# Kernel tuning notes

Hardware: AMD Instinct MI355X
Metric: run time of the kernel (lower is better)

Reference implementation:

```python
import jax, jax.numpy as jnp
import numpy as np

N = 50000      # num nodes
E = 500000     # num edges
R = 200        # num relations
DIN = 128      # ent input dim
DREL = 128     # relation dim
DOUT = 128     # output dim
SLOPE = 0.01   # torch LeakyReLU default negative_slope


def setup_inputs() -> dict:
    key = jax.random.key(0)
    ks = jax.random.split(key, 6)
    x = jax.random.normal(ks[0], (N, DIN), dtype=jnp.float32)
    relation_embedding = jax.random.normal(ks[1], (R, DREL), dtype=jnp.float32)
    edge_index = jax.random.randint(ks[2], (2, E), 0, N, dtype=jnp.int32)
    edge_type = jax.random.randint(ks[3], (E,), 0, R, dtype=jnp.int32)
    # Linear weights (xavier-ish scale), stored as [in, out] for x @ W
    W1 = jax.random.normal(ks[4], (2 * DIN + DREL, DOUT), dtype=jnp.float32) * 0.05
    b1 = jnp.zeros((DOUT,), dtype=jnp.float32)
    w2 = jax.random.normal(ks[5], (DOUT,), dtype=jnp.float32) * 0.05
    return {"x": x, "relation_embedding": relation_embedding, "W1": W1,
            "b1": b1, "w2": w2, "edge_index": edge_index, "edge_type": edge_type}


def reference(x, relation_embedding, W1, b1, w2, edge_index, edge_type):
    src, dst = edge_index[0], edge_index[1]
    n = x.shape[0]
    # gather + concat: [E, 2*DIN + DREL]
    triple = jnp.concatenate([x[src], x[dst], relation_embedding[edge_type]], axis=1)
    c = triple @ W1 + b1                         # [E, DOUT]
    b = jax.nn.leaky_relu(c @ w2, SLOPE)         # [E] attention logits
    # per-destination (segment) softmax — stable, fully vectorized
    seg_max = jax.ops.segment_max(b, dst, num_segments=n)
    ex = jnp.exp(b - seg_max[dst])
    denom = jax.ops.segment_sum(ex, dst, num_segments=n)
    alpha = ex / denom[dst]                      # [E]
    # weighted message scatter-add (dropout p=0 / eval -> identity)
    out = jax.ops.segment_sum(c * alpha[:, None], dst, num_segments=n)  # [N, DOUT]
    # final_layer=False -> leaky_relu on output
    return jax.nn.leaky_relu(out, SLOPE)
```

## Files before the change

kernel.cpp:

```cpp
#include <hip/hip_runtime.h>
#include <math.h>

#define SLOPE 0.01f
#define CHUNK_SHIFT 13
#define CHUNK_SZ (1 << CHUNK_SHIFT)
#define MAXWORDS 12544

using bf16x8 = __attribute__((ext_vector_type(8))) short;
using f32x4  = __attribute__((ext_vector_type(4))) float;

__device__ __forceinline__ unsigned short f2bf(float f) {
  unsigned int u = __float_as_uint(f);
  unsigned int r = 0x7FFFu + ((u >> 16) & 1u);
  return (unsigned short)((u + r) >> 16);
}
__device__ __forceinline__ float bflo(unsigned int v) {
  return __uint_as_float(v << 16);
}
__device__ __forceinline__ float bfhi(unsigned int v) {
  return __uint_as_float(v & 0xFFFF0000u);
}
__device__ __forceinline__ bf16x8 pack8(float4 a, float4 b) {
  bf16x8 r;
  r[0] = (short)f2bf(a.x); r[1] = (short)f2bf(a.y);
  r[2] = (short)f2bf(a.z); r[3] = (short)f2bf(a.w);
  r[4] = (short)f2bf(b.x); r[5] = (short)f2bf(b.y);
  r[6] = (short)f2bf(b.z); r[7] = (short)f2bf(b.w);
  return r;
}

__global__ __launch_bounds__(1024) void front(
    const float* __restrict__ W1, unsigned short* __restrict__ WT,
    const float* __restrict__ rel, const float* __restrict__ b1,
    const float* __restrict__ w2,
    unsigned short* __restrict__ Crelbf, float* __restrict__ pC, int n_rel,
    const int* __restrict__ dsts, unsigned int* __restrict__ cntg,
    unsigned char* __restrict__ rank8, int E, int words, int CB, int WB) {
  __shared__ __align__(16) unsigned int smem[MAXWORDS];
  int b = blockIdx.x;
  int tid = threadIdx.x;
  if (b < CB) {
    for (int w = tid; w < words; w += 1024) smem[w] = 0;
    __syncthreads();
    int base = b << CHUNK_SHIFT;
    int lim = E - base; if (lim > CHUNK_SZ) lim = CHUNK_SZ;
    for (int k = tid; k < lim; k += 1024) {
      int dn = dsts[base + k];
      unsigned int sh = 8u * (dn & 3);
      unsigned int old = atomicAdd(&smem[dn >> 2], 1u << sh);
      rank8[base + k] = (unsigned char)((old >> sh) & 0xFFu);
    }
    __syncthreads();
    unsigned int* dstp = cntg + (size_t)b * words;
    for (int w = tid; w < words; w += 1024) dstp[w] = smem[w];
  } else if (b < CB + WB) {
    int i = (b - CB) * 1024 + tid;
    int n = i >> 7, k = i & 127;
    int src_row = ((n >> 7) << 7) + k;
    WT[n * 128 + k] = f2bf(W1[src_row * 128 + (n & 127)]);
  } else {
    float* rs  = (float*)smem;
    float* red = rs + 1024;
    int h = tid >> 7, d = tid & 127;
    int r = (b - CB - WB) * 8 + h;
    bool valid = r < n_rel;
    rs[h * 128 + d] = valid ? rel[r * 128 + d] : 0.f;
    __syncthreads();
    float acc = b1[d];
    for (int k = 0; k < 128; ++k)
      acc = fmaf(rs[h * 128 + k], W1[(256 + k) * 128 + d], acc);
    if (valid) Crelbf[r * 128 + d] = f2bf(acc);
    red[h * 128 + d] = acc * w2[d];
    __syncthreads();
    for (int s = 64; s > 0; s >>= 1) {
      if (d < s) red[h * 128 + d] += red[h * 128 + d + s];
      __syncthreads();
    }
    if (d == 0 && valid) pC[r] = red[h * 128];
  }
}

__global__ __launch_bounds__(1024, 1) void mid(
    const float* __restrict__ x, const unsigned short* __restrict__ WT,
    const float* __restrict__ w2,
    unsigned short* __restrict__ Abf, unsigned short* __restrict__ Bmbf,
    float* __restrict__ pA, float* __restrict__ pB, int M,
    const unsigned int* __restrict__ cntg, unsigned short* __restrict__ p16,
    int* __restrict__ deg, int* __restrict__ off, int* __restrict__ partial,
    int n, int words, int C, int SB) {
  __shared__ __align__(16) unsigned char smem[65536];
  int b = blockIdx.x;
  int tid = threadIdx.x;

  if (b < SB) {
    int* sdata = (int*)smem;
    int t = tid;
    int i = b * 1024 + t;
    int run = 0;
    if (i < n) {
      int w = i >> 2, sh = 8 * (i & 3);
      for (int c = 0; c < C; ++c) {
        unsigned int cw = cntg[(size_t)c * words + w];
        p16[(size_t)c * n + i] = (unsigned short)run;
        run += (int)((cw >> sh) & 0xFFu);
      }
      deg[i] = run;
    }
    int v = (i < n) ? run : 0;
    sdata[t] = v;
    __syncthreads();
    for (int s = 1; s < 1024; s <<= 1) {
      int add = (t >= s) ? sdata[t - s] : 0;
      __syncthreads();
      sdata[t] += add;
      __syncthreads();
    }
    if (i < n) off[i] = sdata[t] - v;
    if (t == 1023) partial[b] = sdata[1023];
    return;
  }

  #pragma unroll
  for (int j = 0; j < 4; ++j) {
    int idx16 = j * 1024 + tid;
    int nn  = idx16 >> 4;
    int seg = idx16 & 15;
    uint4 v = *(const uint4*)(WT + nn * 128 + seg * 8);
    *(uint4*)(smem + nn * 256 + ((seg * 16) ^ ((nn & 7) << 4))) = v;
  }
  __syncthreads();

  int sub = tid >> 8;
  int t   = tid & 255;
  int m0  = ((b - SB) * 4 + sub) * 64;
  if (m0 >= M) return;

  int wave = t >> 6, lane = t & 63;
  int wm = wave >> 1, wn = wave & 1;
  int l15 = lane & 15, l4 = lane >> 4;

  f32x4 acc[2][8];
  #pragma unroll
  for (int mi = 0; mi < 2; ++mi)
    #pragma unroll
    for (int ni = 0; ni < 8; ++ni) acc[mi][ni] = (f32x4){0.f, 0.f, 0.f, 0.f};

  int arow0 = m0 + wm * 32 + l15;
  int arow1 = arow0 + 16;
  int ar0 = arow0 < M ? arow0 : M - 1;
  int ar1 = arow1 < M ? arow1 : M - 1;
  const float* xbase0 = x + (size_t)ar0 * 128 + l4 * 8;
  const float* xbase1 = x + (size_t)ar1 * 128 + l4 * 8;
  const int nrow = wn * 128 + l15;

  #pragma unroll
  for (int ks = 0; ks < 4; ++ks) {
    float4 a0lo = *(const float4*)(xbase0 + ks * 32);
    float4 a0hi = *(const float4*)(xbase0 + ks * 32 + 4);
    float4 a1lo = *(const float4*)(xbase1 + ks * 32);
    float4 a1hi = *(const float4*)(xbase1 + ks * 32 + 4);
    bf16x8 af0 = pack8(a0lo, a0hi);
    bf16x8 af1 = pack8(a1lo, a1hi);
    int segb = (l4 + ks * 4) * 16;
    #pragma unroll
    for (int ni = 0; ni < 8; ++ni) {
      int nn = nrow + ni * 16;
      bf16x8 bf = *(const bf16x8*)(smem + nn * 256 + (segb ^ ((nn & 7) << 4)));
      acc[0][ni] = __builtin_amdgcn_mfma_f32_16x16x32_bf16(af0, bf, acc[0][ni], 0, 0, 0);
      acc[1][ni] = __builtin_amdgcn_mfma_f32_16x16x32_bf16(af1, bf, acc[1][ni], 0, 0, 0);
    }
  }

  unsigned short* dstp = (wn == 0) ? Abf : Bmbf;
  #pragma unroll
  for (int mi = 0; mi < 2; ++mi) {
    #pragma unroll
    for (int ni = 0; ni < 8; ++ni) {
      int coll = ni * 16 + l15;
      #pragma unroll
      for (int r = 0; r < 4; ++r) {
        int row = m0 + wm * 32 + mi * 16 + l4 * 4 + r;
        if (row < M) dstp[(size_t)row * 128 + coll] = f2bf(acc[mi][ni][r]);
      }
    }
  }

  float w2c[8];
  #pragma unroll
  for (int ni = 0; ni < 8; ++ni) w2c[ni] = w2[ni * 16 + l15];
  float* pdst = (wn == 0) ? pA : pB;
  #pragma unroll
  for (int mi = 0; mi < 2; ++mi) {
    #pragma unroll
    for (int r = 0; r < 4; ++r) {
      float v = 0.f;
      #pragma unroll
      for (int ni = 0; ni < 8; ++ni) v = fmaf(acc[mi][ni][r], w2c[ni], v);
      v += __shfl_xor(v, 1, 64);
      v += __shfl_xor(v, 2, 64);
      v += __shfl_xor(v, 4, 64);
      v += __shfl_xor(v, 8, 64);
      if (l15 == 0) {
        int row = m0 + wm * 32 + mi * 16 + l4 * 4 + r;
        if (row < M) pdst[row] = v;
      }
    }
  }
}

__global__ __launch_bounds__(1024) void fill_perm(
    const int* __restrict__ srcs, const int* __restrict__ dsts,
    const int* __restrict__ types, const unsigned char* __restrict__ rank8,
    const int* __restrict__ off, const int* __restrict__ partial, int nb,
    const unsigned short* __restrict__ p16,
    unsigned int* __restrict__ stperm, int E, int n) {
  __shared__ int carryLUT[64];
  int tid = threadIdx.x;
  if (tid < 64) {
    int v = (tid < nb) ? partial[tid] : 0;
    int inc = v;
    #pragma unroll
    for (int s = 1; s < 64; s <<= 1) {
      int u = __shfl_up(inc, s, 64);
      if (tid >= s) inc += u;
    }
    carryLUT[tid] = inc - v;
  }
  __syncthreads();
  int i = blockIdx.x * 1024 + tid;
  if (i < E) {
    int dn = dsts[i];
    int c = i >> CHUNK_SHIFT;
    int p = off[dn] + carryLUT[dn >> 10] + (int)p16[(size_t)c * n + dn] + (int)rank8[i];
    stperm[p] = (unsigned int)srcs[i] | ((unsigned int)types[i] << 16);
  }
}

__global__ __launch_bounds__(256) void aggregate(
    const int* __restrict__ off, const int* __restrict__ deg,
    const int* __restrict__ partial, int nb,
    const unsigned int* __restrict__ stperm,
    const float* __restrict__ pA, const float* __restrict__ pB,
    const float* __restrict__ pCg,
    const unsigned short* __restrict__ Abf,
    const unsigned short* __restrict__ Bmbf,
    const unsigned short* __restrict__ Crelbf,
    float* __restrict__ out, int n_nodes, int n_rel) {
  __shared__ float pCs[256];
  __shared__ int carryLUT[64];
  int tid = threadIdx.x;
  if (tid < 64) {
    int v = (tid < nb) ? partial[tid] : 0;
    int inc = v;
    #pragma unroll
    for (int s = 1; s < 64; s <<= 1) {
      int u = __shfl_up(inc, s, 64);
      if (tid >= s) inc += u;
    }
    carryLUT[tid] = inc - v;
  }
  for (int r = tid; r < n_rel; r += 256) pCs[r] = pCg[r];
  __syncthreads();

  int n = blockIdx.x * 16 + (tid >> 4);
  if (n >= n_nodes) return;
  int lane = tid & 15;
  int c8 = lane * 8;
  int start = off[n] + carryLUT[n >> 10];
  int dcnt = deg[n];
  size_t obase = (size_t)n * 128 + c8;
  if (dcnt == 0) {
    *(float4*)(out + obase)     = (float4){0.f, 0.f, 0.f, 0.f};
    *(float4*)(out + obase + 4) = (float4){0.f, 0.f, 0.f, 0.f};
    return;
  }
  float pBn = pB[n];
  float a0 = 0.f, a1 = 0.f, a2 = 0.f, a3 = 0.f;
  float a4 = 0.f, a5 = 0.f, a6 = 0.f, a7 = 0.f, S = 0.f;
  int i = 0;
  for (; i + 4 <= dcnt; i += 4) {
    unsigned int st[4];
    #pragma unroll
    for (int j = 0; j < 4; ++j) st[j] = stperm[start + i + j];
    uint4 av[4], cv[4];
    float pa[4];
    #pragma unroll
    for (int j = 0; j < 4; ++j) {
      unsigned int s = st[j] & 0xFFFFu, t = st[j] >> 16;
      av[j] = *(const uint4*)(Abf + ((size_t)s << 7) + c8);
      cv[j] = *(const uint4*)(Crelbf + (t << 7) + c8);
      pa[j] = pA[s];
    }
    #pragma unroll
    for (int j = 0; j < 4; ++j) {
      float b = pa[j] + pBn + pCs[st[j] >> 16];
      b = b > 0.f ? b : SLOPE * b;
      float ex = __expf(b);
      S += ex;
      a0 = fmaf(ex, bflo(av[j].x) + bflo(cv[j].x), a0);
      a1 = fmaf(ex, bfhi(av[j].x) + bfhi(cv[j].x), a1);
      a2 = fmaf(ex, bflo(av[j].y) + bflo(cv[j].y), a2);
      a3 = fmaf(ex, bfhi(av[j].y) + bfhi(cv[j].y), a3);
      a4 = fmaf(ex, bflo(av[j].z) + bflo(cv[j].z), a4);
      a5 = fmaf(ex, bfhi(av[j].z) + bfhi(cv[j].z), a5);
      a6 = fmaf(ex, bflo(av[j].w) + bflo(cv[j].w), a6);
      a7 = fmaf(ex, bfhi(av[j].w) + bfhi(cv[j].w), a7);
    }
  }
  for (; i < dcnt; ++i) {
    unsigned int st = stperm[start + i];
    unsigned int s = st & 0xFFFFu, t = st >> 16;
    uint4 av = *(const uint4*)(Abf + ((size_t)s << 7) + c8);
    uint4 cv = *(const uint4*)(Crelbf + (t << 7) + c8);
    float b = pA[s] + pBn + pCs[t];
    b = b > 0.f ? b : SLOPE * b;
    float ex = __expf(b);
    S += ex;
    a0 = fmaf(ex, bflo(av.x) + bflo(cv.x), a0);
    a1 = fmaf(ex, bfhi(av.x) + bfhi(cv.x), a1);
    a2 = fmaf(ex, bflo(av.y) + bflo(cv.y), a2);
    a3 = fmaf(ex, bfhi(av.y) + bfhi(cv.y), a3);
    a4 = fmaf(ex, bflo(av.z) + bflo(cv.z), a4);
    a5 = fmaf(ex, bfhi(av.z) + bfhi(cv.z), a5);
    a6 = fmaf(ex, bflo(av.w) + bflo(cv.w), a6);
    a7 = fmaf(ex, bfhi(av.w) + bfhi(cv.w), a7);
  }
  float inv = 1.f / S;
  uint4 bm = *(const uint4*)(Bmbf + obase);
  float o0 = a0 * inv + bflo(bm.x);
  float o1 = a1 * inv + bfhi(bm.x);
  float o2 = a2 * inv + bflo(bm.y);
  float o3 = a3 * inv + bfhi(bm.y);
  float o4 = a4 * inv + bflo(bm.z);
  float o5 = a5 * inv + bfhi(bm.z);
  float o6 = a6 * inv + bflo(bm.w);
  float o7 = a7 * inv + bfhi(bm.w);
  o0 = o0 > 0.f ? o0 : SLOPE * o0;
  o1 = o1 > 0.f ? o1 : SLOPE * o1;
  o2 = o2 > 0.f ? o2 : SLOPE * o2;
  o3 = o3 > 0.f ? o3 : SLOPE * o3;
  o4 = o4 > 0.f ? o4 : SLOPE * o4;
  o5 = o5 > 0.f ? o5 : SLOPE * o5;
  o6 = o6 > 0.f ? o6 : SLOPE * o6;
  o7 = o7 > 0.f ? o7 : SLOPE * o7;
  *(float4*)(out + obase)     = (float4){o0, o1, o2, o3};
  *(float4*)(out + obase + 4) = (float4){o4, o5, o6, o7};
}

extern "C" void kernel_launch(void* const* d_in, const int* in_sizes, int n_in,
                              void* d_out, int out_size, void* d_ws, size_t ws_size,
                              hipStream_t stream) {
  const float* x    = (const float*)d_in[0];
  const float* rel  = (const float*)d_in[1];
  const float* W1   = (const float*)d_in[2];
  const float* b1   = (const float*)d_in[3];
  const float* w2   = (const float*)d_in[4];
  const int* edge_index = (const int*)d_in[5];
  const int* edge_type  = (const int*)d_in[6];

  int n_nodes = in_sizes[0] / 128;
  int n_rel   = in_sizes[1] / 128;
  int E       = in_sizes[6];
  const int* srcs = edge_index;
  const int* dsts = edge_index + E;
  float* out = (float*)d_out;

  int words = (n_nodes + 3) >> 2;
  int C     = (E + CHUNK_SZ - 1) >> CHUNK_SHIFT;

  auto align256 = [](size_t v) { return (v + 255) & ~(size_t)255; };
  char* ws = (char*)d_ws;
  unsigned short* WT     = (unsigned short*)ws; ws += align256(256 * 128 * 2);
  unsigned short* Abf    = (unsigned short*)ws; ws += align256((size_t)n_nodes * 128 * 2);
  unsigned short* Bmbf   = (unsigned short*)ws; ws += align256((size_t)n_nodes * 128 * 2);
  unsigned short* Crelbf = (unsigned short*)ws; ws += align256((size_t)n_rel * 128 * 2);
  float* pA    = (float*)ws; ws += align256((size_t)n_nodes * 4);
  float* pB    = (float*)ws; ws += align256((size_t)n_nodes * 4);
  float* pC    = (float*)ws; ws += align256((size_t)n_rel * 4);
  int* deg     = (int*)ws;   ws += align256((size_t)n_nodes * 4);
  int* off     = (int*)ws;   ws += align256((size_t)n_nodes * 4);
  int* partial = (int*)ws;   ws += align256(1024 * 4);
  unsigned int* cntg = (unsigned int*)ws;    ws += align256((size_t)C * words * 4);
  unsigned short* p16 = (unsigned short*)ws; ws += align256((size_t)C * n_nodes * 2);
  unsigned char* rank8 = (unsigned char*)ws; ws += align256((size_t)E);
  unsigned int* stperm = (unsigned int*)ws;  ws += align256((size_t)E * 4);

  int CB = C;
  int WB = 32;
  int RB = (n_rel + 7) / 8;
  front<<<CB + WB + RB, 1024, 0, stream>>>(
      W1, WT, rel, b1, w2, Crelbf, pC, n_rel,
      dsts, cntg, rank8, E, words, CB, WB);

  int nb = (n_nodes + 1023) / 1024;
  int gB = (n_nodes + 63) / 64;
  int gB4 = (gB + 3) / 4;
  mid<<<nb + gB4, 1024, 0, stream>>>(
      x, WT, w2, Abf, Bmbf, pA, pB, n_nodes,
      cntg, p16, deg, off, partial, n_nodes, words, C, nb);

  fill_perm<<<(E + 1023) / 1024, 1024, 0, stream>>>(
      srcs, dsts, edge_type, rank8, off, partial, nb, p16, stperm, E, n_nodes);

  aggregate<<<(n_nodes + 15) / 16, 256, 0, stream>>>(
      off, deg, partial, nb, stperm, pA, pB, pC, Abf, Bmbf, Crelbf,
      out, n_nodes, n_rel);
}
```

Baseline: 78.78 us.

## Split scan into own kernel and co-launch GEMM with permutation fill

```diff
diff --git a/kernel.cpp b/kernel.cpp
--- a/kernel.cpp
+++ b/kernel.cpp
@@ -80,43 +80,70 @@
   }
 }
 
-__global__ __launch_bounds__(1024, 1) void mid(
+__global__ __launch_bounds__(1024) void scan_p16(
+    const unsigned int* __restrict__ cntg, unsigned short* __restrict__ p16,
+    int* __restrict__ deg, int* __restrict__ off, int* __restrict__ partial,
+    int n, int words, int C) {
+  __shared__ int sdata[1024];
+  int t = threadIdx.x;
+  int i = blockIdx.x * 1024 + t;
+  int run = 0;
+  if (i < n) {
+    int w = i >> 2, sh = 8 * (i & 3);
+    for (int c = 0; c < C; ++c) {
+      unsigned int cw = cntg[(size_t)c * words + w];
+      p16[(size_t)c * n + i] = (unsigned short)run;
+      run += (int)((cw >> sh) & 0xFFu);
+    }
+    deg[i] = run;
+  }
+  int v = (i < n) ? run : 0;
+  sdata[t] = v;
+  __syncthreads();
+  for (int s = 1; s < 1024; s <<= 1) {
+    int add = (t >= s) ? sdata[t - s] : 0;
+    __syncthreads();
+    sdata[t] += add;
+    __syncthreads();
+  }
+  if (i < n) off[i] = sdata[t] - v;
+  if (t == 1023) partial[blockIdx.x] = sdata[1023];
+}
+
+__global__ __launch_bounds__(1024, 1) void work(
     const float* __restrict__ x, const unsigned short* __restrict__ WT,
     const float* __restrict__ w2,
     unsigned short* __restrict__ Abf, unsigned short* __restrict__ Bmbf,
-    float* __restrict__ pA, float* __restrict__ pB, int M,
-    const unsigned int* __restrict__ cntg, unsigned short* __restrict__ p16,
-    int* __restrict__ deg, int* __restrict__ off, int* __restrict__ partial,
-    int n, int words, int C, int SB) {
+    float* __restrict__ pA, float* __restrict__ pB, int M, int GB,
+    const int* __restrict__ srcs, const int* __restrict__ dsts,
+    const int* __restrict__ types, const unsigned char* __restrict__ rank8,
+    const int* __restrict__ off, const int* __restrict__ partial, int nb,
+    const unsigned short* __restrict__ p16,
+    unsigned int* __restrict__ stperm, int E, int n) {
   __shared__ __align__(16) unsigned char smem[65536];
   int b = blockIdx.x;
   int tid = threadIdx.x;
 
-  if (b < SB) {
-    int* sdata = (int*)smem;
-    int t = tid;
-    int i = b * 1024 + t;
-    int run = 0;
-    if (i < n) {
-      int w = i >> 2, sh = 8 * (i & 3);
-      for (int c = 0; c < C; ++c) {
-        unsigned int cw = cntg[(size_t)c * words + w];
-        p16[(size_t)c * n + i] = (unsigned short)run;
-        run += (int)((cw >> sh) & 0xFFu);
+  if (b >= GB) {
+    int* carryLUT = (int*)smem;
+    if (tid < 64) {
+      int v = (tid < nb) ? partial[tid] : 0;
+      int inc = v;
+      #pragma unroll
+      for (int s = 1; s < 64; s <<= 1) {
+        int u = __shfl_up(inc, s, 64);
+        if (tid >= s) inc += u;
       }
-      deg[i] = run;
-    }
-    int v = (i < n) ? run : 0;
-    sdata[t] = v;
-    __syncthreads();
-    for (int s = 1; s < 1024; s <<= 1) {
-      int add = (t >= s) ? sdata[t - s] : 0;
-      __syncthreads();
-      sdata[t] += add;
-      __syncthreads();
-    }
-    if (i < n) off[i] = sdata[t] - v;
-    if (t == 1023) partial[b] = sdata[1023];
+      carryLUT[tid] = inc - v;
+    }
+    __syncthreads();
+    int i = (b - GB) * 1024 + tid;
+    if (i < E) {
+      int dn = dsts[i];
+      int c = i >> CHUNK_SHIFT;
+      int p = off[dn] + carryLUT[dn >> 10] + (int)p16[(size_t)c * n + dn] + (int)rank8[i];
+      stperm[p] = (unsigned int)srcs[i] | ((unsigned int)types[i] << 16);
+    }
     return;
   }
 
@@ -132,7 +159,7 @@
 
   int sub = tid >> 8;
   int t   = tid & 255;
-  int m0  = ((b - SB) * 4 + sub) * 64;
+  int m0  = (b * 4 + sub) * 64;
   if (m0 >= M) return;
 
   int wave = t >> 6, lane = t & 63;
@@ -205,34 +232,6 @@
         if (row < M) pdst[row] = v;
       }
     }
-  }
-}
-
-__global__ __launch_bounds__(1024) void fill_perm(
-    const int* __restrict__ srcs, const int* __restrict__ dsts,
-    const int* __restrict__ types, const unsigned char* __restrict__ rank8,
-    const int* __restrict__ off, const int* __restrict__ partial, int nb,
-    const unsigned short* __restrict__ p16,
-    unsigned int* __restrict__ stperm, int E, int n) {
-  __shared__ int carryLUT[64];
-  int tid = threadIdx.x;
-  if (tid < 64) {
-    int v = (tid < nb) ? partial[tid] : 0;
-    int inc = v;
-    #pragma unroll
-    for (int s = 1; s < 64; s <<= 1) {
-      int u = __shfl_up(inc, s, 64);
-      if (tid >= s) inc += u;
-    }
-    carryLUT[tid] = inc - v;
-  }
-  __syncthreads();
-  int i = blockIdx.x * 1024 + tid;
-  if (i < E) {
-    int dn = dsts[i];
-    int c = i >> CHUNK_SHIFT;
-    int p = off[dn] + carryLUT[dn >> 10] + (int)p16[(size_t)c * n + dn] + (int)rank8[i];
-    stperm[p] = (unsigned int)srcs[i] | ((unsigned int)types[i] << 16);
   }
 }
 
@@ -393,13 +392,14 @@
       dsts, cntg, rank8, E, words, CB, WB);
 
   int nb = (n_nodes + 1023) / 1024;
+  scan_p16<<<nb, 1024, 0, stream>>>(cntg, p16, deg, off, partial,
+                                    n_nodes, words, C);
+
   int gB = (n_nodes + 63) / 64;
-  int gB4 = (gB + 3) / 4;
-  mid<<<nb + gB4, 1024, 0, stream>>>(
-      x, WT, w2, Abf, Bmbf, pA, pB, n_nodes,
-      cntg, p16, deg, off, partial, n_nodes, words, C, nb);
-
-  fill_perm<<<(E + 1023) / 1024, 1024, 0, stream>>>(
+  int GB = (gB + 3) / 4;
+  int fB = (E + 1023) / 1024;
+  work<<<GB + fB, 1024, 0, stream>>>(
+      x, WT, w2, Abf, Bmbf, pA, pB, n_nodes, GB,
       srcs, dsts, edge_type, rank8, off, partial, nb, p16, stperm, E, n_nodes);
 
   aggregate<<<(n_nodes + 15) / 16, 256, 0, stream>>>(
```

Result: slower. 89.86 us (+14.1%).
